# Kernel tuning notes

Measured on AMD Instinct MI355X. Metric: run time of the kernel, lower is better.

Reference implementation:

```python
import jax, jax.numpy as jnp
import numpy as np

K_IN = 9      # input_patch_size
K_OUT = 3     # output_patch_size
C_IN = 4      # nb_of_input_features
C_OUT = 2     # nb_of_output_features
HID = 50      # int_layer_width
B, H, W = 16, 128, 128
CUT = K_IN // 2 - K_OUT // 2  # border pixels cut from output (3)


def _unfold(x, k):
    # x: [B, C, H, W] -> [B, C*k*k, L] with torch unfold ordering (c, ki, kj)
    b, c, h, w = x.shape
    ho, wo = h - k + 1, w - k + 1
    cols = jnp.stack([x[:, :, i:i + ho, j:j + wo]
                      for i in range(k) for j in range(k)], axis=2)  # [B,C,k*k,ho,wo]
    return cols.reshape(b, c * k * k, ho * wo)


def _fold_add(patches, oh, ow):
    # patches: [B, C, k, k, ho, wo] -> overlap-add into [B, C, oh, ow]
    b, c, k, _, ho, wo = patches.shape
    out = jnp.zeros((b, c, oh, ow), dtype=patches.dtype)
    for i in range(k):
        for j in range(k):
            out = out.at[:, :, i:i + ho, j:j + wo].add(patches[:, :, i, j])
    return out


def setup_inputs() -> dict:
    key = jax.random.key(0)
    ks = jax.random.split(key, 7)
    f_in = C_IN * K_IN * K_IN      # 324
    f_out = C_OUT * K_OUT * K_OUT  # 18
    s1 = 1.0 / np.sqrt(f_in)
    s2 = 1.0 / np.sqrt(HID)
    return {
        "x": jax.random.normal(ks[0], (B, C_IN, H, W), dtype=jnp.float32),
        "W1": jax.random.uniform(ks[1], (f_in, HID), jnp.float32, -s1, s1),
        "b1": jax.random.uniform(ks[2], (HID,), jnp.float32, -s1, s1),
        "W2": jax.random.uniform(ks[3], (HID, HID), jnp.float32, -s2, s2),
        "b2": jax.random.uniform(ks[4], (HID,), jnp.float32, -s2, s2),
        "W3": jax.random.uniform(ks[5], (HID, f_out), jnp.float32, -s2, s2),
        "b3": jax.random.uniform(ks[6], (f_out,), jnp.float32, -s2, s2),
    }


def reference(x, W1, b1, W2, b2, W3, b3):
    b, c, h, w = x.shape
    oh, ow = h - 2 * CUT, w - 2 * CUT          # 122, 122
    ho, wo = h - K_IN + 1, w - K_IN + 1        # 120, 120 (= oh-K_OUT+1)
    # unfold -> [B, L, C_in*K_in^2] -> flatten rows
    cols = _unfold(x, K_IN)                    # [B, 324, L]
    feats = cols.transpose(0, 2, 1).reshape(b * ho * wo, -1)
    # 3-layer MLP
    hmid = jax.nn.relu(feats @ W1 + b1)
    hmid = jax.nn.relu(hmid @ W2 + b2)
    out = hmid @ W3 + b3                       # [B*L, C_out*K_out^2]
    # fold (overlap-add), torch feature ordering (c, ki, kj)
    patches = out.reshape(b, ho, wo, C_OUT, K_OUT, K_OUT)
    patches = patches.transpose(0, 3, 4, 5, 1, 2)  # [B, C_out, k, k, ho, wo]
    res = _fold_add(patches, oh, ow)
    # divisor = fold(unfold(ones)) -> per-pixel overlap count
    ones_patches = jnp.ones((1, 1, K_OUT, K_OUT, ho, wo), dtype=x.dtype)
    divisor = _fold_add(ones_patches, oh, ow)  # [1,1,oh,ow]
    return res / divisor
```

## Files before the change

### kernel.cpp

```cpp
#include <hip/hip_runtime.h>
#include <hip/hip_bf16.h>

#define BATCH   16
#define C_INF   4
#define H_IN    128
#define W_IN    128
#define HID     50
#define F_OUT   18
#define HO      120
#define WO      120
#define OH      122
#define OW      122
#define NPOS    (BATCH * HO * WO)
#define MBLK    128
#define NBLKS   (NPOS / MBLK)

#define NB1     (11*4*64*8)
#define NB2     (2*4*64*8)
#define NB3     (2*2*64*8)
#define NWF     (NB1 + NB2 + NB3)
#define WOFF    (NPOS * F_OUT)
#define NXC     (BATCH * C_INF * H_IN * W_IN)
#define PREP_BLOCKS  ((NWF + 255) / 256)
#define XCONV_BLOCKS (NXC / (256 * 8))
#define CW      16
#define NSTG    (36*512)

typedef float    v4f     __attribute__((ext_vector_type(4)));
typedef short    short4v __attribute__((ext_vector_type(4)));
typedef short    short8  __attribute__((ext_vector_type(8)));
typedef _Float16 v8hf    __attribute__((ext_vector_type(8)));
typedef int      v4i     __attribute__((ext_vector_type(4)));
typedef short8 short8_a4 __attribute__((aligned(4)));

__device__ inline short f2h(float x) {
    _Float16 h = (_Float16)x;
    return __builtin_bit_cast(short, h);
}
__device__ inline float h2f(short s) {
    return (float)__builtin_bit_cast(_Float16, s);
}

__device__ inline int hswz(int m, int j) {
    return (m * 64 + j) ^ ((m & 7) << 3);
}

__device__ inline int slot_to_k1(int s, int qb, int e) {
    if (s < 9) {
        int pair = s*4 + qb;
        int c = pair/9, ki = pair - c*9;
        return c*81 + ki*9 + e;
    }
    int r = (s-9)*32 + qb*8 + e;
    if (r >= 36) return -1;
    int c = r/9, ki = r - c*9;
    return c*81 + ki*9 + 8;
}

__global__ __launch_bounds__(256)
void prep_kernel(const float* __restrict__ x,
                 const float* __restrict__ W1, const float* __restrict__ W2,
                 const float* __restrict__ W3, short* __restrict__ wf,
                 short* __restrict__ xe, short* __restrict__ xo)
{
    const int blk = blockIdx.x;
    if (blk >= PREP_BLOCKS) {
        const int j = ((blk - PREP_BLOCKS)*256 + (int)threadIdx.x) * 8;
        v4f a = *(const v4f*)&x[j];
        v4f b = *(const v4f*)&x[j + 4];
        float c9 = (j + 8 < NXC) ? x[j + 8] : 0.f;
        short s[9];
        #pragma unroll
        for (int e = 0; e < 4; ++e) { s[e] = f2h(a[e]); s[e+4] = f2h(b[e]); }
        s[8] = f2h(c9);
        short8 ve, vo;
        #pragma unroll
        for (int e = 0; e < 8; ++e) { ve[e] = s[e]; vo[e] = s[e+1]; }
        *(short8*)&xe[j] = ve;
        *(short8*)&xo[j] = vo;
        return;
    }
    int i = blk * 256 + threadIdx.x;
    if (i >= NWF) return;
    float val;
    if (i < NB1) {
        int t = i;
        int e = t & 7, lane = (t >> 3) & 63;
        int rest = t >> 9;
        int u = rest & 3, s = rest >> 2;
        int k = slot_to_k1(s, lane >> 4, e);
        int n = u*16 + (lane & 15);
        val = (k >= 0 && n < HID) ? W1[k*HID + n] : 0.f;
    } else if (i < NB1 + NB2) {
        int t = i - NB1;
        int e = t & 7, lane = (t >> 3) & 63;
        int rest = t >> 9;
        int u = rest & 3, s = rest >> 2;
        int k = s*32 + ((lane >> 4) << 3) + e;
        int n = u*16 + (lane & 15);
        val = (k < HID && n < HID) ? W2[k*HID + n] : 0.f;
    } else {
        int t = i - NB1 - NB2;
        int e = t & 7, lane = (t >> 3) & 63;
        int rest = t >> 9;
        int u = rest & 1, s = rest >> 1;
        int k = s*32 + ((lane >> 4) << 3) + e;
        int n = u*16 + (lane & 15);
        val = (k < HID && n < F_OUT) ? W3[k*F_OUT + n] : 0.f;
    }
    wf[i] = f2h(val);
}

__global__ __launch_bounds__(256, 3)
void mfma_mlp(const short* __restrict__ xe, const short* __restrict__ xo,
              const float* __restrict__ b1, const float* __restrict__ b2,
              const float* __restrict__ b3,
              const short* __restrict__ wf, short* __restrict__ out3)
{
    __shared__ short wlds[NSTG];
    __shared__ short h_lds[128 * 64];

    const int tid  = threadIdx.x;
    const int lane = tid & 63;
    const int w    = tid >> 6;
    const int q    = lane >> 4, col = lane & 15;
    const int mbase = blockIdx.x * MBLK;
    const int mw    = w * 32;

    #pragma unroll
    for (int it = 0; it < 9; ++it) {
        const int cbase = it*256 + w*64;
        const short* g  = wf + (cbase + lane)*8;
        __builtin_amdgcn_global_load_lds(
            (const __attribute__((address_space(1))) void*)g,
            (__attribute__((address_space(3))) void*)&wlds[cbase*8],
            16, 0, 0);
    }

    float bias1[4], bias2[4], bias3[2];
    #pragma unroll
    for (int u = 0; u < 4; ++u) {
        int j = u*16 + col;
        bias1[u] = (j < HID) ? b1[j] : 0.f;
        bias2[u] = (j < HID) ? b2[j] : 0.f;
    }
    #pragma unroll
    for (int u = 0; u < 2; ++u) {
        int j = u*16 + col;
        bias3[u] = (j < F_OUT) ? b3[j] : 0.f;
    }

    const short* xp[2];
    #pragma unroll
    for (int t = 0; t < 2; ++t) {
        int pos = mbase + mw + t*16 + col;
        int b   = pos / (HO*WO); int rem = pos - b*(HO*WO);
        int y   = rem / WO;      int xc  = rem - y*WO;
        int bi  = b*(C_INF*H_IN*W_IN) + y*W_IN + xc;
        xp[t] = (bi & 1) ? (xo + (bi - 1)) : (xe + bi);
    }

    const v4i* B1L = (const v4i*)wf + lane;
    const v4i* B2L = (const v4i*)(wf + NB1) + lane;
    const v4i* B3L = (const v4i*)(wf + NB1 + NB2) + lane;

    __syncthreads();

    v4f acc[2][4];
    #pragma unroll
    for (int t = 0; t < 2; ++t)
        #pragma unroll
        for (int u = 0; u < 4; ++u)
            acc[t][u] = (v4f){0.f, 0.f, 0.f, 0.f};

    #pragma unroll
    for (int s = 0; s < 9; ++s) {
        const int pair = s*4 + q;
        const int c = pair/9, ki = pair - c*9;
        const int off = c*(H_IN*W_IN) + ki*W_IN;

        short8 ah[2];
        #pragma unroll
        for (int t = 0; t < 2; ++t)
            ah[t] = *(const short8_a4*)(xp[t] + off);

        #pragma unroll
        for (int u = 0; u < 4; ++u) {
            v4i bv = *(const v4i*)&wlds[((s*4 + u)*64 + lane)*8];
            v8hf bh = __builtin_bit_cast(v8hf, bv);
            #pragma unroll
            for (int t = 0; t < 2; ++t) {
                v8hf a_h = __builtin_bit_cast(v8hf, ah[t]);
                acc[t][u] = __builtin_amdgcn_mfma_f32_16x16x32_f16(a_h, bh, acc[t][u], 0, 0, 0);
            }
        }
    }
    #pragma unroll
    for (int sr = 0; sr < 2; ++sr) {
        const int s = 9 + sr;
        short8 ah[2];
        #pragma unroll
        for (int e = 0; e < 8; ++e) {
            int r = sr*32 + q*8 + e;
            bool valid = (r < 36);
            int c = valid ? r/9 : 0;
            int ki = r - c*9;
            int off = c*(H_IN*W_IN) + ki*W_IN + 8;
            #pragma unroll
            for (int t = 0; t < 2; ++t)
                ah[t][e] = valid ? xp[t][off] : (short)0;
        }
        #pragma unroll
        for (int u = 0; u < 4; ++u) {
            v8hf bh = __builtin_bit_cast(v8hf, B1L[(s*4 + u)*64]);
            #pragma unroll
            for (int t = 0; t < 2; ++t) {
                v8hf a_h = __builtin_bit_cast(v8hf, ah[t]);
                acc[t][u] = __builtin_amdgcn_mfma_f32_16x16x32_f16(a_h, bh, acc[t][u], 0, 0, 0);
            }
        }
    }

    #pragma unroll
    for (int u = 0; u < 4; ++u) {
        #pragma unroll
        for (int t = 0; t < 2; ++t) {
            #pragma unroll
            for (int r = 0; r < 4; ++r) {
                float v = fmaxf(acc[t][u][r] + bias1[u], 0.f);
                int m = mw + t*16 + q*4 + r;
                h_lds[hswz(m, u*16 + col)] = f2h(v);
            }
        }
    }

    v4f acc2[2][4];
    #pragma unroll
    for (int t = 0; t < 2; ++t)
        #pragma unroll
        for (int u = 0; u < 4; ++u)
            acc2[t][u] = (v4f){0.f, 0.f, 0.f, 0.f};

    #pragma unroll
    for (int s = 0; s < 2; ++s) {
        short8 ah2[2];
        #pragma unroll
        for (int t = 0; t < 2; ++t) {
            int m = mw + t*16 + col;
            ah2[t] = *(const short8*)&h_lds[hswz(m, s*32 + q*8)];
        }
        #pragma unroll
        for (int u = 0; u < 4; ++u) {
            v8hf bh = __builtin_bit_cast(v8hf, B2L[(s*4 + u)*64]);
            #pragma unroll
            for (int t = 0; t < 2; ++t) {
                v8hf a_h = __builtin_bit_cast(v8hf, ah2[t]);
                acc2[t][u] = __builtin_amdgcn_mfma_f32_16x16x32_f16(a_h, bh, acc2[t][u], 0, 0, 0);
            }
        }
    }

    #pragma unroll
    for (int u = 0; u < 4; ++u) {
        #pragma unroll
        for (int t = 0; t < 2; ++t) {
            #pragma unroll
            for (int r = 0; r < 4; ++r) {
                float v = fmaxf(acc2[t][u][r] + bias2[u], 0.f);
                int m = mw + t*16 + q*4 + r;
                h_lds[hswz(m, u*16 + col)] = f2h(v);
            }
        }
    }

    v4f acc3[2][2];
    #pragma unroll
    for (int t = 0; t < 2; ++t)
        #pragma unroll
        for (int u = 0; u < 2; ++u)
            acc3[t][u] = (v4f){0.f, 0.f, 0.f, 0.f};

    #pragma unroll
    for (int s = 0; s < 2; ++s) {
        short8 ah3[2];
        #pragma unroll
        for (int t = 0; t < 2; ++t) {
            int m = mw + t*16 + col;
            ah3[t] = *(const short8*)&h_lds[hswz(m, s*32 + q*8)];
        }
        #pragma unroll
        for (int u = 0; u < 2; ++u) {
            v8hf bh = __builtin_bit_cast(v8hf, B3L[(s*2 + u)*64]);
            #pragma unroll
            for (int t = 0; t < 2; ++t) {
                v8hf a_h = __builtin_bit_cast(v8hf, ah3[t]);
                acc3[t][u] = __builtin_amdgcn_mfma_f32_16x16x32_f16(a_h, bh, acc3[t][u], 0, 0, 0);
            }
        }
    }

    #pragma unroll
    for (int u = 0; u < 2; ++u) {
        int j = u*16 + col;
        if (j < F_OUT) {
            #pragma unroll
            for (int t = 0; t < 2; ++t) {
                short4v vs;
                #pragma unroll
                for (int r = 0; r < 4; ++r) vs[r] = f2h(acc3[t][u][r] + bias3[u]);
                *(short4v*)&out3[j*NPOS + mbase + mw + t*16 + q*4] = vs;
            }
        }
    }
}

__global__ __launch_bounds__(256)
void fold_kernel(const short* __restrict__ out3, float* __restrict__ out)
{
    const int idx = blockIdx.x * 256 + threadIdx.x;
    const int total = BATCH * 2 * OH * CW;
    if (idx >= total) return;

    int t = idx;
    const int cx = t % CW; t /= CW;
    const int oy = t % OH; t /= OH;
    const int c  = t & 1;  t >>= 1;
    const int b  = t;
    const int ox0 = cx * 8;

    if (oy >= 2 && oy < HO && cx >= 1 && cx <= 14) {
        float accv[8];
        #pragma unroll
        for (int e = 0; e < 8; ++e) accv[e] = 0.f;
        #pragma unroll
        for (int ki = 0; ki < 3; ++ki) {
            const int y    = oy - ki;
            const int rowb = (b*HO + y)*WO;
            const int ob   = (c*3 + ki)*3;
            short8 v0 = *(const short8_a4*)&out3[(ob + 0)*NPOS + rowb + ox0];
            short8 v1 = *(const short8_a4*)&out3[(ob + 1)*NPOS + rowb + ox0 - 2];
            int   v1b = *(const int*)      &out3[(ob + 1)*NPOS + rowb + ox0 + 6];
            short8 v2 = *(const short8_a4*)&out3[(ob + 2)*NPOS + rowb + ox0 - 2];
            #pragma unroll
            for (int e = 0; e < 8; ++e) {
                accv[e] += h2f(v0[e]);
                accv[e] += (e < 7) ? h2f(v1[e + 1]) : h2f((short)(v1b & 0xffff));
                accv[e] += h2f(v2[e]);
            }
        }
        float* op = &out[((b*2 + c)*OH + oy)*OW + ox0];
        #pragma unroll
        for (int e = 0; e < 8; ++e) op[e] = accv[e] / 9.f;
        return;
    }

    #pragma unroll
    for (int e = 0; e < 8; ++e) {
        const int ox = ox0 + e;
        if (ox < OW) {
            const int ylo = max(0, oy - 2), yhi = min(HO - 1, oy);
            const int xlo = max(0, ox - 2), xhi = min(WO - 1, ox);
            float s = 0.f;
            for (int y = ylo; y <= yhi; ++y) {
                const int ki = oy - y;
                for (int xx = xlo; xx <= xhi; ++xx) {
                    const int kj = ox - xx;
                    const int o  = (c*3 + ki)*3 + kj;
                    s += h2f(out3[o*NPOS + (b*HO + y)*WO + xx]);
                }
            }
            const float div = (float)((yhi - ylo + 1) * (xhi - xlo + 1));
            out[((b*2 + c)*OH + oy)*OW + ox] = s / div;
        }
    }
}

extern "C" void kernel_launch(void* const* d_in, const int* in_sizes, int n_in,
                              void* d_out, int out_size, void* d_ws, size_t ws_size,
                              hipStream_t stream)
{
    const float* x  = (const float*)d_in[0];
    const float* W1 = (const float*)d_in[1];
    const float* b1 = (const float*)d_in[2];
    const float* W2 = (const float*)d_in[3];
    const float* b2 = (const float*)d_in[4];
    const float* W3 = (const float*)d_in[5];
    const float* b3 = (const float*)d_in[6];

    short* out3 = (short*)d_ws;
    short* wf   = out3 + WOFF;
    short* xe   = wf + NWF;
    short* xo   = xe + NXC;

    prep_kernel<<<PREP_BLOCKS + XCONV_BLOCKS, 256, 0, stream>>>(x, W1, W2, W3, wf, xe, xo);

    mfma_mlp<<<NBLKS, 256, 0, stream>>>(xe, xo, b1, b2, b3, wf, out3);

    const int total = BATCH * 2 * OH * CW;
    fold_kernel<<<(total + 255) / 256, 256, 0, stream>>>(out3, (float*)d_out);
}
```

Before: 114.6 us.

## Make MLP kernel persistent with hoisted input loads and interleaved chunk order

```diff
diff --git a/kernel.cpp b/kernel.cpp
--- a/kernel.cpp
+++ b/kernel.cpp
@@ -13,7 +13,8 @@
 #define OW      122
 #define NPOS    (BATCH * HO * WO)
 #define MBLK    128
-#define NBLKS   (NPOS / MBLK)
+#define NCH     (NPOS / MBLK)
+#define GBLK    600
 
 #define NB1     (11*4*64*8)
 #define NB2     (2*4*64*8)
@@ -40,9 +41,16 @@
 __device__ inline float h2f(short s) {
     return (float)__builtin_bit_cast(_Float16, s);
 }
+__device__ inline void keepv(short8 x) {
+    asm volatile("" :: "v"(__builtin_bit_cast(v4i, x)));
+}
 
 __device__ inline int hswz(int m, int j) {
     return (m * 64 + j) ^ ((m & 7) << 3);
+}
+
+__device__ inline int chunk_base(int c) {
+    return (((c & 7) * (NCH / 8)) + (c >> 3)) * MBLK;
 }
 
 __device__ inline int slot_to_k1(int s, int qb, int e) {
@@ -124,8 +132,7 @@
     const int lane = tid & 63;
     const int w    = tid >> 6;
     const int q    = lane >> 4, col = lane & 15;
-    const int mbase = blockIdx.x * MBLK;
-    const int mw    = w * 32;
+    const int mw   = w * 32;
 
     #pragma unroll
     for (int it = 0; it < 9; ++it) {
@@ -150,165 +157,180 @@
         bias3[u] = (j < F_OUT) ? b3[j] : 0.f;
     }
 
-    const short* xp[2];
-    #pragma unroll
-    for (int t = 0; t < 2; ++t) {
-        int pos = mbase + mw + t*16 + col;
-        int b   = pos / (HO*WO); int rem = pos - b*(HO*WO);
-        int y   = rem / WO;      int xc  = rem - y*WO;
-        int bi  = b*(C_INF*H_IN*W_IN) + y*W_IN + xc;
-        xp[t] = (bi & 1) ? (xo + (bi - 1)) : (xe + bi);
-    }
-
     const v4i* B1L = (const v4i*)wf + lane;
     const v4i* B2L = (const v4i*)(wf + NB1) + lane;
     const v4i* B3L = (const v4i*)(wf + NB1 + NB2) + lane;
 
     __syncthreads();
 
-    v4f acc[2][4];
-    #pragma unroll
-    for (int t = 0; t < 2; ++t)
-        #pragma unroll
-        for (int u = 0; u < 4; ++u)
-            acc[t][u] = (v4f){0.f, 0.f, 0.f, 0.f};
-
-    #pragma unroll
-    for (int s = 0; s < 9; ++s) {
-        const int pair = s*4 + q;
-        const int c = pair/9, ki = pair - c*9;
-        const int off = c*(H_IN*W_IN) + ki*W_IN;
-
-        short8 ah[2];
+    #pragma unroll 1
+    for (int ch = blockIdx.x; ch < NCH; ch += GBLK) {
+        const int mb = chunk_base(ch);
+
+        const short* xp[2];
+        #pragma unroll
+        for (int t = 0; t < 2; ++t) {
+            int pos = mb + mw + t*16 + col;
+            int b   = pos / (HO*WO); int rem = pos - b*(HO*WO);
+            int y   = rem / WO;      int xc  = rem - y*WO;
+            int bi  = b*(C_INF*H_IN*W_IN) + y*W_IN + xc;
+            xp[t] = (bi & 1) ? (xo + (bi - 1)) : (xe + bi);
+        }
+
+        short8 ah[9][2];
+        #pragma unroll
+        for (int s = 0; s < 9; ++s) {
+            const int pair = s*4 + q;
+            const int c = pair/9, ki = pair - c*9;
+            const int off = c*(H_IN*W_IN) + ki*W_IN;
+            #pragma unroll
+            for (int t = 0; t < 2; ++t)
+                ah[s][t] = *(const short8_a4*)(xp[t] + off);
+        }
+        short8 ahr[2][2];
+        #pragma unroll
+        for (int sr = 0; sr < 2; ++sr) {
+            #pragma unroll
+            for (int e = 0; e < 8; ++e) {
+                int r = sr*32 + q*8 + e;
+                bool valid = (r < 36);
+                int c = valid ? r/9 : 0;
+                int ki = r - c*9;
+                int off = c*(H_IN*W_IN) + ki*W_IN + 8;
+                #pragma unroll
+                for (int t = 0; t < 2; ++t)
+                    ahr[sr][t][e] = valid ? xp[t][off] : (short)0;
+            }
+        }
+        #pragma unroll
+        for (int s = 0; s < 9; ++s) { keepv(ah[s][0]); keepv(ah[s][1]); }
+        #pragma unroll
+        for (int sr = 0; sr < 2; ++sr) { keepv(ahr[sr][0]); keepv(ahr[sr][1]); }
+
+        v4f acc[2][4];
         #pragma unroll
         for (int t = 0; t < 2; ++t)
-            ah[t] = *(const short8_a4*)(xp[t] + off);
+            #pragma unroll
+            for (int u = 0; u < 4; ++u)
+                acc[t][u] = (v4f){0.f, 0.f, 0.f, 0.f};
+
+        #pragma unroll
+        for (int s = 0; s < 9; ++s) {
+            #pragma unroll
+            for (int u = 0; u < 4; ++u) {
+                v4i bv = *(const v4i*)&wlds[((s*4 + u)*64 + lane)*8];
+                v8hf bh = __builtin_bit_cast(v8hf, bv);
+                #pragma unroll
+                for (int t = 0; t < 2; ++t) {
+                    v8hf a_h = __builtin_bit_cast(v8hf, ah[s][t]);
+                    acc[t][u] = __builtin_amdgcn_mfma_f32_16x16x32_f16(a_h, bh, acc[t][u], 0, 0, 0);
+                }
+            }
+        }
+        #pragma unroll
+        for (int sr = 0; sr < 2; ++sr) {
+            const int s = 9 + sr;
+            #pragma unroll
+            for (int u = 0; u < 4; ++u) {
+                v8hf bh = __builtin_bit_cast(v8hf, B1L[(s*4 + u)*64]);
+                #pragma unroll
+                for (int t = 0; t < 2; ++t) {
+                    v8hf a_h = __builtin_bit_cast(v8hf, ahr[sr][t]);
+                    acc[t][u] = __builtin_amdgcn_mfma_f32_16x16x32_f16(a_h, bh, acc[t][u], 0, 0, 0);
+                }
+            }
+        }
 
         #pragma unroll
         for (int u = 0; u < 4; ++u) {
-            v4i bv = *(const v4i*)&wlds[((s*4 + u)*64 + lane)*8];
-            v8hf bh = __builtin_bit_cast(v8hf, bv);
             #pragma unroll
             for (int t = 0; t < 2; ++t) {
-                v8hf a_h = __builtin_bit_cast(v8hf, ah[t]);
-                acc[t][u] = __builtin_amdgcn_mfma_f32_16x16x32_f16(a_h, bh, acc[t][u], 0, 0, 0);
-            }
-        }
-    }
-    #pragma unroll
-    for (int sr = 0; sr < 2; ++sr) {
-        const int s = 9 + sr;
-        short8 ah[2];
-        #pragma unroll
-        for (int e = 0; e < 8; ++e) {
-            int r = sr*32 + q*8 + e;
-            bool valid = (r < 36);
-            int c = valid ? r/9 : 0;
-            int ki = r - c*9;
-            int off = c*(H_IN*W_IN) + ki*W_IN + 8;
-            #pragma unroll
-            for (int t = 0; t < 2; ++t)
-                ah[t][e] = valid ? xp[t][off] : (short)0;
-        }
+                #pragma unroll
+                for (int r = 0; r < 4; ++r) {
+                    float v = fmaxf(acc[t][u][r] + bias1[u], 0.f);
+                    int m = mw + t*16 + q*4 + r;
+                    h_lds[hswz(m, u*16 + col)] = f2h(v);
+                }
+            }
+        }
+
+        v4f acc2[2][4];
+        #pragma unroll
+        for (int t = 0; t < 2; ++t)
+            #pragma unroll
+            for (int u = 0; u < 4; ++u)
+                acc2[t][u] = (v4f){0.f, 0.f, 0.f, 0.f};
+
+        #pragma unroll
+        for (int s = 0; s < 2; ++s) {
+            short8 ah2[2];
+            #pragma unroll
+            for (int t = 0; t < 2; ++t) {
+                int m = mw + t*16 + col;
+                ah2[t] = *(const short8*)&h_lds[hswz(m, s*32 + q*8)];
+            }
+            #pragma unroll
+            for (int u = 0; u < 4; ++u) {
+                v8hf bh = __builtin_bit_cast(v8hf, B2L[(s*4 + u)*64]);
+                #pragma unroll
+                for (int t = 0; t < 2; ++t) {
+                    v8hf a_h = __builtin_bit_cast(v8hf, ah2[t]);
+                    acc2[t][u] = __builtin_amdgcn_mfma_f32_16x16x32_f16(a_h, bh, acc2[t][u], 0, 0, 0);
+                }
+            }
+        }
+
         #pragma unroll
         for (int u = 0; u < 4; ++u) {
-            v8hf bh = __builtin_bit_cast(v8hf, B1L[(s*4 + u)*64]);
             #pragma unroll
             for (int t = 0; t < 2; ++t) {
-                v8hf a_h = __builtin_bit_cast(v8hf, ah[t]);
-                acc[t][u] = __builtin_amdgcn_mfma_f32_16x16x32_f16(a_h, bh, acc[t][u], 0, 0, 0);
-            }
-        }
-    }
-
-    #pragma unroll
-    for (int u = 0; u < 4; ++u) {
-        #pragma unroll
-        for (int t = 0; t < 2; ++t) {
-            #pragma unroll
-            for (int r = 0; r < 4; ++r) {
-                float v = fmaxf(acc[t][u][r] + bias1[u], 0.f);
-                int m = mw + t*16 + q*4 + r;
-                h_lds[hswz(m, u*16 + col)] = f2h(v);
-            }
-        }
-    }
-
-    v4f acc2[2][4];
-    #pragma unroll
-    for (int t = 0; t < 2; ++t)
-        #pragma unroll
-        for (int u = 0; u < 4; ++u)
-            acc2[t][u] = (v4f){0.f, 0.f, 0.f, 0.f};
-
-    #pragma unroll
-    for (int s = 0; s < 2; ++s) {
-        short8 ah2[2];
-        #pragma unroll
-        for (int t = 0; t < 2; ++t) {
-            int m = mw + t*16 + col;
-            ah2[t] = *(const short8*)&h_lds[hswz(m, s*32 + q*8)];
-        }
-        #pragma unroll
-        for (int u = 0; u < 4; ++u) {
-            v8hf bh = __builtin_bit_cast(v8hf, B2L[(s*4 + u)*64]);
+                #pragma unroll
+                for (int r = 0; r < 4; ++r) {
+                    float v = fmaxf(acc2[t][u][r] + bias2[u], 0.f);
+                    int m = mw + t*16 + q*4 + r;
+                    h_lds[hswz(m, u*16 + col)] = f2h(v);
+                }
+            }
+        }
+
+        v4f acc3[2][2];
+        #pragma unroll
+        for (int t = 0; t < 2; ++t)
+            #pragma unroll
+            for (int u = 0; u < 2; ++u)
+                acc3[t][u] = (v4f){0.f, 0.f, 0.f, 0.f};
+
+        #pragma unroll
+        for (int s = 0; s < 2; ++s) {
+            short8 ah3[2];
             #pragma unroll
             for (int t = 0; t < 2; ++t) {
-                v8hf a_h = __builtin_bit_cast(v8hf, ah2[t]);
-                acc2[t][u] = __builtin_amdgcn_mfma_f32_16x16x32_f16(a_h, bh, acc2[t][u], 0, 0, 0);
-            }
-        }
-    }
-
-    #pragma unroll
-    for (int u = 0; u < 4; ++u) {
-        #pragma unroll
-        for (int t = 0; t < 2; ++t) {
-            #pragma unroll
-            for (int r = 0; r < 4; ++r) {
-                float v = fmaxf(acc2[t][u][r] + bias2[u], 0.f);
-                int m = mw + t*16 + q*4 + r;
-                h_lds[hswz(m, u*16 + col)] = f2h(v);
-            }
-        }
-    }
-
-    v4f acc3[2][2];
-    #pragma unroll
-    for (int t = 0; t < 2; ++t)
-        #pragma unroll
-        for (int u = 0; u < 2; ++u)
-            acc3[t][u] = (v4f){0.f, 0.f, 0.f, 0.f};
-
-    #pragma unroll
-    for (int s = 0; s < 2; ++s) {
-        short8 ah3[2];
-        #pragma unroll
-        for (int t = 0; t < 2; ++t) {
-            int m = mw + t*16 + col;
-            ah3[t] = *(const short8*)&h_lds[hswz(m, s*32 + q*8)];
-        }
+                int m = mw + t*16 + col;
+                ah3[t] = *(const short8*)&h_lds[hswz(m, s*32 + q*8)];
+            }
+            #pragma unroll
+            for (int u = 0; u < 2; ++u) {
+                v8hf bh = __builtin_bit_cast(v8hf, B3L[(s*2 + u)*64]);
+                #pragma unroll
+                for (int t = 0; t < 2; ++t) {
+                    v8hf a_h = __builtin_bit_cast(v8hf, ah3[t]);
+                    acc3[t][u] = __builtin_amdgcn_mfma_f32_16x16x32_f16(a_h, bh, acc3[t][u], 0, 0, 0);
+                }
+            }
+        }
+
         #pragma unroll
         for (int u = 0; u < 2; ++u) {
-            v8hf bh = __builtin_bit_cast(v8hf, B3L[(s*2 + u)*64]);
-            #pragma unroll
-            for (int t = 0; t < 2; ++t) {
-                v8hf a_h = __builtin_bit_cast(v8hf, ah3[t]);
-                acc3[t][u] = __builtin_amdgcn_mfma_f32_16x16x32_f16(a_h, bh, acc3[t][u], 0, 0, 0);
-            }
-        }
-    }
-
-    #pragma unroll
-    for (int u = 0; u < 2; ++u) {
-        int j = u*16 + col;
-        if (j < F_OUT) {
-            #pragma unroll
-            for (int t = 0; t < 2; ++t) {
-                short4v vs;
-                #pragma unroll
-                for (int r = 0; r < 4; ++r) vs[r] = f2h(acc3[t][u][r] + bias3[u]);
-                *(short4v*)&out3[j*NPOS + mbase + mw + t*16 + q*4] = vs;
+            int j = u*16 + col;
+            if (j < F_OUT) {
+                #pragma unroll
+                for (int t = 0; t < 2; ++t) {
+                    short4v vs;
+                    #pragma unroll
+                    for (int r = 0; r < 4; ++r) vs[r] = f2h(acc3[t][u][r] + bias3[u]);
+                    __builtin_nontemporal_store(vs,
+                        (short4v*)&out3[j*NPOS + mb + mw + t*16 + q*4]);
+                }
             }
         }
     }
@@ -394,7 +416,7 @@
 
     prep_kernel<<<PREP_BLOCKS + XCONV_BLOCKS, 256, 0, stream>>>(x, W1, W2, W3, wf, xe, xo);
 
-    mfma_mlp<<<NBLKS, 256, 0, stream>>>(xe, xo, b1, b2, b3, wf, out3);
+    mfma_mlp<<<GBLK, 256, 0, stream>>>(xe, xo, b1, b2, b3, wf, out3);
 
     const int total = BATCH * 2 * OH * CW;
     fold_kernel<<<(total + 255) / 256, 256, 0, stream>>>(out3, (float*)d_out);
```

Result: slower. 147.2 us (+28.5%).
